# Kernel tuning notes

Hardware: AMD Instinct MI355X
Metric: run time of the kernel (lower is better)

The kernel has to match this reference:

```python
import jax, jax.numpy as jnp
import numpy as np

RADIUS = 1.0      # cfg['radius']
NEAR = 0.5        # cfg['near']
N_STEPS = 32      # cfg['ray_marching_steps']
N_SECANT = 8      # n_secant_steps in unisurf()
TAU = 0.5         # occupancy decision threshold
EPS = 1e-6        # module-level epsilon


def _occ(p, W1, b1, W2, b2):
    # stand-in occupancy network: [..., 3] -> [...]
    h = jax.nn.relu(p @ W1 + b1)
    return jax.nn.sigmoid(h @ W2 + b2)[..., 0]


def get_sphere_intersection(cam_loc, rays, r=RADIUS):
    # cam_loc: [B,3], rays: [B,P,3] (unit). Faithful to the torch version.
    ray_cam_dot = jnp.einsum('bpd,bd->bp', rays, cam_loc)                    # [B,P]
    under_sqrt = ray_cam_dot ** 2 - (jnp.sum(cam_loc ** 2, -1, keepdims=True) - r * r)
    mask_intersect = under_sqrt > 0
    s = jnp.sqrt(jnp.where(mask_intersect, under_sqrt, 0.0))
    inter = jnp.stack([-s - ray_cam_dot, s - ray_cam_dot], axis=-1)          # [B,P,2]
    inter = jnp.where(mask_intersect[..., None], inter, 0.0)
    return jnp.maximum(inter, 0.0), mask_intersect


def setup_inputs() -> dict:
    key = jax.random.key(0)
    k1, k2, k3, k4, k5, k6 = jax.random.split(key, 6)
    B, P, H = 1, 131072, 32
    # camera ~2 units from origin; rays aimed at points near the unit sphere
    cam_loc = jnp.array([[0.0, 0.0, 2.0]], dtype=jnp.float32) + 0.01 * jax.random.normal(k1, (B, 3))
    targets = 0.3 * jax.random.normal(k2, (B, P, 3))
    ray_directions = (targets - cam_loc[:, None, :]).astype(jnp.float32)
    W1 = (0.8 * jax.random.normal(k3, (3, H))).astype(jnp.float32)
    b1 = (0.1 * jax.random.normal(k4, (H,))).astype(jnp.float32)
    W2 = (0.5 * jax.random.normal(k5, (H, 1))).astype(jnp.float32)
    b2 = (0.1 * jax.random.normal(k6, (1,))).astype(jnp.float32)
    return {"cam_loc": cam_loc, "ray_directions": ray_directions,
            "W1": W1, "b1": b1, "W2": W2, "b2": b2}


def reference(cam_loc, ray_directions, W1, b1, W2, b2):
    rays = ray_directions / jnp.linalg.norm(ray_directions, axis=-1, keepdims=True)
    inter, mask_int = get_sphere_intersection(cam_loc, rays, RADIUS)
    far = jnp.maximum(inter[..., 1], NEAR + EPS)                             # [B,P]

    # coarse march: N_STEPS samples per ray between near and sphere-far
    t = jnp.linspace(0.0, 1.0, N_STEPS, dtype=jnp.float32)                   # [S]
    d = NEAR * (1.0 - t) + far[..., None] * t                                # [B,P,S]
    p = cam_loc[:, None, None, :] + rays[:, :, None, :] * d[..., None]       # [B,P,S,3]
    f = _occ(p, W1, b1, W2, b2) - TAU                                        # [B,P,S]

    # first free->occupied sign change (masked-index pattern, vectorized)
    cross = (f[..., :-1] < 0) & (f[..., 1:] >= 0)                            # [B,P,S-1]
    found = jnp.any(cross, axis=-1) & mask_int                               # [B,P]
    idx = jnp.argmax(cross, axis=-1)                                         # [B,P]

    def take(a, i):
        return jnp.take_along_axis(a, i[..., None], axis=-1)[..., 0]

    d_low, f_low = take(d, idx), take(f, idx)
    d_high, f_high = take(d, idx + 1), take(f, idx + 1)

    def secant_body(_, c):
        dl, fl, dh, fh = c
        den = fh - fl
        den = jnp.where(jnp.abs(den) < EPS, EPS, den)
        dm = dl - fl * (dh - dl) / den
        pm = cam_loc[:, None, :] + rays * dm[..., None]
        fm = _occ(pm, W1, b1, W2, b2) - TAU
        neg = fm < 0
        return (jnp.where(neg, dm, dl), jnp.where(neg, fm, fl),
                jnp.where(neg, dh, dm), jnp.where(neg, fh, fm))

    d_low, f_low, d_high, f_high = jax.lax.fori_loop(
        0, N_SECANT, secant_body, (d_low, f_low, d_high, f_high))
    den = f_high - f_low
    den = jnp.where(jnp.abs(den) < EPS, EPS, den)
    d_mid = d_low - f_low * (d_high - d_low) / den
    d_pred = jnp.where(found, d_mid, 0.0)                                    # [B,P]

    # surface points fed back to the model (depth detached, as in torch)
    p_surf = cam_loc[:, None, :] + rays * jax.lax.stop_gradient(d_pred)[..., None]
    occ_surf = jnp.where(found, _occ(p_surf, W1, b1, W2, b2), 0.0)           # [B,P]
    return d_pred, occ_surf
```

## Files before the change

### kernel.cpp

```cpp
#include <hip/hip_runtime.h>
#include <math.h>

#define HDIM 32
#define NSTEPS 32
#define NSECANT 8
#define RADIUSV 1.0f
#define NEARV 0.5f
#define TAUV 0.5f
#define EPSV 1e-6f

typedef float f2 __attribute__((ext_vector_type(2)));

__device__ __forceinline__ unsigned pair_other_u(unsigned x) {
    return (unsigned)__builtin_amdgcn_ds_swizzle((int)x, 0x041F);
}

__global__ __launch_bounds__(256) void unisurf_kernel(
    const float* __restrict__ cam_loc,
    const float* __restrict__ ray_dirs,
    const float* __restrict__ W1,
    const float* __restrict__ b1,
    const float* __restrict__ W2,
    const float* __restrict__ b2,
    float* __restrict__ out,
    int P)
{
    __shared__ float4 sW[HDIM];
    __shared__ float  sW2[HDIM];
    __shared__ float  sB2;

    const int tid = threadIdx.x;
    if (tid < HDIM) {
        sW[tid] = make_float4(W1[tid], W1[HDIM + tid], W1[2 * HDIM + tid], b1[tid]);
        sW2[tid] = W2[tid];
    }
    if (tid == 0) sB2 = b2[0];
    __syncthreads();

    const int j = blockIdx.x * blockDim.x + tid;
    const int r = j >> 1;
    if (r >= P) return;
    const int sub = j & 1;

    const float cx = cam_loc[0], cy = cam_loc[1], cz = cam_loc[2];

    float dx = ray_dirs[3 * r + 0];
    float dy = ray_dirs[3 * r + 1];
    float dz = ray_dirs[3 * r + 2];
    float nrm = sqrtf(dx * dx + dy * dy + dz * dz);
    float rx = dx / nrm, ry = dy / nrm, rz = dz / nrm;

    float rcd = rx * cx + ry * cy + rz * cz;
    float c2  = cx * cx + cy * cy + cz * cz;
    float us  = rcd * rcd - (c2 - RADIUSV * RADIUSV);
    bool  mask_int = us > 0.0f;
    float s_sq = mask_int ? sqrtf(us) : 0.0f;
    float far_raw = mask_int ? fmaxf(s_sq - rcd, 0.0f) : 0.0f;
    float farv = fmaxf(far_raw, NEARV + EPSV);

    f2 rW[HDIM / 2], cW[HDIM / 2], w2[HDIM / 2];
    #pragma unroll
    for (int h = 0; h < HDIM / 2; ++h) {
        float4 wa = sW[2 * h], wb = sW[2 * h + 1];
        rW[h] = (f2){rx * wa.x + ry * wa.y + rz * wa.z,
                     rx * wb.x + ry * wb.y + rz * wb.z};
        cW[h] = (f2){cx * wa.x + cy * wa.y + cz * wa.z + wa.w,
                     cx * wb.x + cy * wb.y + cz * wb.z + wb.w};
        w2[h] = (f2){sW2[2 * h], sW2[2 * h + 1]};
    }
    const float B2 = sB2;
    const f2 z2 = (f2){0.0f, 0.0f};

    auto logit = [&](float d) -> float {
        f2 dv = (f2){d, d};
        f2 a0 = z2, a1 = z2, a2 = z2, a3 = z2;
        #pragma unroll
        for (int h = 0; h < HDIM / 2; h += 4) {
            f2 x0 = __builtin_elementwise_fma(dv, rW[h + 0], cW[h + 0]);
            f2 x1 = __builtin_elementwise_fma(dv, rW[h + 1], cW[h + 1]);
            f2 x2 = __builtin_elementwise_fma(dv, rW[h + 2], cW[h + 2]);
            f2 x3 = __builtin_elementwise_fma(dv, rW[h + 3], cW[h + 3]);
            a0 = __builtin_elementwise_fma(__builtin_elementwise_max(x0, z2), w2[h + 0], a0);
            a1 = __builtin_elementwise_fma(__builtin_elementwise_max(x1, z2), w2[h + 1], a1);
            a2 = __builtin_elementwise_fma(__builtin_elementwise_max(x2, z2), w2[h + 2], a2);
            a3 = __builtin_elementwise_fma(__builtin_elementwise_max(x3, z2), w2[h + 3], a3);
        }
        f2 aa = (a0 + a1) + (a2 + a3);
        return (aa.x + aa.y) + B2;
    };
    auto sigm = [](float x) -> float {
        float e = __expf(-x);
        return __builtin_amdgcn_rcpf(1.0f + e);
    };

    const float STEPC = 0.03225806451612903f;

    unsigned msk = 0u;
    #pragma unroll
    for (int k = 0; k < 16; ++k) {
        float t = (float)(sub + 2 * k) * STEPC;
        float dd = NEARV * (1.0f - t) + farv * t;
        float ls = logit(dd);
        msk |= (ls >= 0.0f) ? (1u << k) : 0u;
    }

    unsigned om = pair_other_u(msk);
    unsigned E = sub ? om : msk;
    unsigned O = sub ? msk : om;

    unsigned candE = (~E & O) & 0xFFFFu;
    unsigned candO = (~O & (E >> 1)) & 0x7FFFu;
    int sE = candE ? 2 * __builtin_ctz(candE) : 1000;
    int sO = candO ? 2 * __builtin_ctz(candO) + 1 : 1000;
    int sstar = sE < sO ? sE : sO;
    bool found = sstar < 1000;
    if (!found) sstar = 0;
    found = found && mask_int;

    float tlo = (float)sstar * STEPC;
    float thi = (float)(sstar + 1) * STEPC;
    float d_lo = NEARV * (1.0f - tlo) + farv * tlo;
    float d_hi = NEARV * (1.0f - thi) + farv * thi;
    float f_lo = sigm(logit(d_lo)) - TAUV;
    float f_hi = sigm(logit(d_hi)) - TAUV;

    #pragma unroll 1
    for (int it = 0; it < NSECANT; ++it) {
        float den = f_hi - f_lo;
        den = (fabsf(den) < EPSV) ? EPSV : den;
        float dm = d_lo - f_lo * (d_hi - d_lo) * __builtin_amdgcn_rcpf(den);
        float fm = sigm(logit(dm)) - TAUV;
        bool neg = fm < 0.0f;
        d_lo = neg ? dm : d_lo;
        f_lo = neg ? fm : f_lo;
        d_hi = neg ? d_hi : dm;
        f_hi = neg ? f_hi : fm;
    }
    float den = f_hi - f_lo;
    den = (fabsf(den) < EPSV) ? EPSV : den;
    float d_mid = d_lo - f_lo * (d_hi - d_lo) * __builtin_amdgcn_rcpf(den);

    float d_pred = found ? d_mid : 0.0f;
    float occ_s = sigm(logit(d_pred));
    float occ_surf = found ? occ_s : 0.0f;

    if (sub == 0) out[r] = d_pred;
    else          out[P + r] = occ_surf;
}

extern "C" void kernel_launch(void* const* d_in, const int* in_sizes, int n_in,
                              void* d_out, int out_size, void* d_ws, size_t ws_size,
                              hipStream_t stream) {
    const float* cam_loc  = (const float*)d_in[0];
    const float* ray_dirs = (const float*)d_in[1];
    const float* W1       = (const float*)d_in[2];
    const float* b1       = (const float*)d_in[3];
    const float* W2       = (const float*)d_in[4];
    const float* b2       = (const float*)d_in[5];
    float* out = (float*)d_out;

    const int P = in_sizes[1] / 3;
    const int block = 256;
    const long long total = 2LL * P;
    const int grid = (int)((total + block - 1) / block);
    unisurf_kernel<<<grid, block, 0, stream>>>(cam_loc, ray_dirs, W1, b1, W2, b2, out, P);
}
```

Measured before the change: 23.98 us.

## Process one ray per thread with paired logit evaluation instead of two-lane split

Moves from two threads per ray (each doing half the coarse samples, then exchanging masks via ds_swizzle) to one thread per ray doing all 32 coarse samples. Two depth samples are evaluated together per MLP pass to raise instruction-level parallelism. The coarse loop is no longer unrolled, and launch bounds now request 2 blocks per CU. This removes the duplicated per-ray setup, secant and final work that both lanes of a pair used to run, at the cost of half as many threads and a longer serial chain per thread.

```diff
diff --git a/kernel.cpp b/kernel.cpp
--- a/kernel.cpp
+++ b/kernel.cpp
@@ -11,11 +11,7 @@
 
 typedef float f2 __attribute__((ext_vector_type(2)));
 
-__device__ __forceinline__ unsigned pair_other_u(unsigned x) {
-    return (unsigned)__builtin_amdgcn_ds_swizzle((int)x, 0x041F);
-}
-
-__global__ __launch_bounds__(256) void unisurf_kernel(
+__global__ __launch_bounds__(256, 2) void unisurf_kernel(
     const float* __restrict__ cam_loc,
     const float* __restrict__ ray_dirs,
     const float* __restrict__ W1,
@@ -37,10 +33,8 @@
     if (tid == 0) sB2 = b2[0];
     __syncthreads();
 
-    const int j = blockIdx.x * blockDim.x + tid;
-    const int r = j >> 1;
+    const int r = blockIdx.x * blockDim.x + tid;
     if (r >= P) return;
-    const int sub = j & 1;
 
     const float cx = cam_loc[0], cy = cam_loc[1], cz = cam_loc[2];
 
@@ -71,6 +65,24 @@
     const float B2 = sB2;
     const f2 z2 = (f2){0.0f, 0.0f};
 
+    auto logit2 = [&](float dA, float dB, float& lA, float& lB) {
+        f2 dvA = (f2){dA, dA}, dvB = (f2){dB, dB};
+        f2 aA0 = z2, aA1 = z2, aB0 = z2, aB1 = z2;
+        #pragma unroll
+        for (int h = 0; h < HDIM / 2; h += 2) {
+            f2 xA0 = __builtin_elementwise_fma(dvA, rW[h + 0], cW[h + 0]);
+            f2 xB0 = __builtin_elementwise_fma(dvB, rW[h + 0], cW[h + 0]);
+            f2 xA1 = __builtin_elementwise_fma(dvA, rW[h + 1], cW[h + 1]);
+            f2 xB1 = __builtin_elementwise_fma(dvB, rW[h + 1], cW[h + 1]);
+            aA0 = __builtin_elementwise_fma(__builtin_elementwise_max(xA0, z2), w2[h + 0], aA0);
+            aB0 = __builtin_elementwise_fma(__builtin_elementwise_max(xB0, z2), w2[h + 0], aB0);
+            aA1 = __builtin_elementwise_fma(__builtin_elementwise_max(xA1, z2), w2[h + 1], aA1);
+            aB1 = __builtin_elementwise_fma(__builtin_elementwise_max(xB1, z2), w2[h + 1], aB1);
+        }
+        f2 sA = aA0 + aA1, sB = aB0 + aB1;
+        lA = (sA.x + sA.y) + B2;
+        lB = (sB.x + sB.y) + B2;
+    };
     auto logit = [&](float d) -> float {
         f2 dv = (f2){d, d};
         f2 a0 = z2, a1 = z2, a2 = z2, a3 = z2;
@@ -96,33 +108,32 @@
     const float STEPC = 0.03225806451612903f;
 
     unsigned msk = 0u;
-    #pragma unroll
+    #pragma unroll 1
     for (int k = 0; k < 16; ++k) {
-        float t = (float)(sub + 2 * k) * STEPC;
-        float dd = NEARV * (1.0f - t) + farv * t;
-        float ls = logit(dd);
-        msk |= (ls >= 0.0f) ? (1u << k) : 0u;
+        float tA = (float)k * STEPC;
+        float tB = (float)(k + 16) * STEPC;
+        float dA = NEARV * (1.0f - tA) + farv * tA;
+        float dB = NEARV * (1.0f - tB) + farv * tB;
+        float lA, lB;
+        logit2(dA, dB, lA, lB);
+        unsigned bA = (lA >= 0.0f) ? (1u << k) : 0u;
+        unsigned bB = (lB >= 0.0f) ? (1u << (k + 16)) : 0u;
+        msk |= bA | bB;
     }
 
-    unsigned om = pair_other_u(msk);
-    unsigned E = sub ? om : msk;
-    unsigned O = sub ? msk : om;
-
-    unsigned candE = (~E & O) & 0xFFFFu;
-    unsigned candO = (~O & (E >> 1)) & 0x7FFFu;
-    int sE = candE ? 2 * __builtin_ctz(candE) : 1000;
-    int sO = candO ? 2 * __builtin_ctz(candO) + 1 : 1000;
-    int sstar = sE < sO ? sE : sO;
-    bool found = sstar < 1000;
-    if (!found) sstar = 0;
+    unsigned cand = (~msk & (msk >> 1)) & 0x7FFFFFFFu;
+    bool found = cand != 0u;
+    int sstar = found ? __builtin_ctz(cand) : 0;
     found = found && mask_int;
 
     float tlo = (float)sstar * STEPC;
     float thi = (float)(sstar + 1) * STEPC;
     float d_lo = NEARV * (1.0f - tlo) + farv * tlo;
     float d_hi = NEARV * (1.0f - thi) + farv * thi;
-    float f_lo = sigm(logit(d_lo)) - TAUV;
-    float f_hi = sigm(logit(d_hi)) - TAUV;
+    float lLo, lHi;
+    logit2(d_lo, d_hi, lLo, lHi);
+    float f_lo = sigm(lLo) - TAUV;
+    float f_hi = sigm(lHi) - TAUV;
 
     #pragma unroll 1
     for (int it = 0; it < NSECANT; ++it) {
@@ -144,8 +155,8 @@
     float occ_s = sigm(logit(d_pred));
     float occ_surf = found ? occ_s : 0.0f;
 
-    if (sub == 0) out[r] = d_pred;
-    else          out[P + r] = occ_surf;
+    out[r]     = d_pred;
+    out[P + r] = occ_surf;
 }
 
 extern "C" void kernel_launch(void* const* d_in, const int* in_sizes, int n_in,
@@ -161,7 +172,6 @@
 
     const int P = in_sizes[1] / 3;
     const int block = 256;
-    const long long total = 2LL * P;
-    const int grid = (int)((total + block - 1) / block);
+    const int grid = (P + block - 1) / block;
     unisurf_kernel<<<grid, block, 0, stream>>>(cam_loc, ray_dirs, W1, b1, W2, b2, out, P);
 }
```

Measured after the change: 19.84 us. -17.3%, faster.
